# Kernel tuning notes

Measured on AMD Instinct MI355X. Metric: run time of the kernel, lower is better.

Reference implementation:

```python
import jax, jax.numpy as jnp
import numpy as np

N_NODES = 150000  # num_users + num_items
EMB_DIM = 64
N_EDGES = 4000000


def setup_inputs() -> dict:
    key = jax.random.key(0)
    k1, k2 = jax.random.split(key)
    x = jax.random.normal(k1, (N_NODES, EMB_DIM), dtype=jnp.float32)
    edge_index = jax.random.randint(k2, (2, N_EDGES), 0, N_NODES, dtype=jnp.int64)
    return {"x": x, "edge_index": edge_index}


def _lgconv(x, row, col, w):
    # message: x[row] * w ; aggregate: scatter-add into col
    msg = x[row] * w[:, None]  # [E, D]
    return jax.ops.segment_sum(msg, col, num_segments=N_NODES)


def reference(x, edge_index):
    row, col = edge_index[0], edge_index[1]
    # gcn_norm without self-loops: deg from target index (col)
    deg = jax.ops.segment_sum(jnp.ones(row.shape[0], x.dtype), col,
                              num_segments=N_NODES)
    dis = jnp.where(deg > 0, jax.lax.rsqrt(jnp.maximum(deg, 1.0)), 0.0)
    w = dis[row] * dis[col]  # [E]

    emb0 = x
    emb1 = _lgconv(emb0, row, col, w)
    emb2 = _lgconv(emb1, row, col, w)
    # stack over layer dim then mean == mean of the three layer embeddings
    out = (emb0 + emb1 + emb2) / 3.0
    return out
```

## Files before the change

### kernel.cpp

```cpp
#include <hip/hip_runtime.h>
#include <hip/hip_bf16.h>


#define EMB_DIM 64
#define BUCKET_BITS 9
#define BUCKET_SZ 512
#define EPB 8192
#define NBMAX 512
#define CAP 16384
#define GSTRIDE 16

typedef float f32x4 __attribute__((ext_vector_type(4)));

__device__ __forceinline__ float bf_lo(unsigned int q) { return __uint_as_float(q << 16); }
__device__ __forceinline__ float bf_hi(unsigned int q) { return __uint_as_float(q & 0xffff0000u); }
__device__ __forceinline__ unsigned int f2bf(float f) {
    unsigned int u = __float_as_uint(f);
    return (u + 0x7fffu + ((u >> 16) & 1u)) >> 16;
}

__global__ void init_kernel(int* __restrict__ gcur, int NB) {
    int t = threadIdx.x;
    if (t < NB) gcur[t * GSTRIDE] = t * CAP;
}

__global__ void fused_scatter(const int* __restrict__ rows,
                              const int* __restrict__ cols,
                              int* __restrict__ gcur,
                              unsigned int* __restrict__ pairs,
                              int E, int NB) {
    __shared__ unsigned int sbuf[EPB];
    __shared__ unsigned short sbkt[EPB];
    __shared__ int lh[NBMAX];
    __shared__ int lexc[NBMAX];
    __shared__ int lbase[NBMAX];
    __shared__ int lrank[NBMAX];
    __shared__ int sc[NBMAX];
    int blk = blockIdx.x, t = threadIdx.x;
    for (int b = t; b < NBMAX; b += 1024) lh[b] = 0;
    __syncthreads();
    int start = blk * EPB, end = min(start + EPB, E);
    int nloc = end - start;
    int myc[8], myr[8];
#pragma unroll
    for (int j = 0; j < 8; ++j) {
        int i = start + t + j * 1024;
        if (i < end) {
            myc[j] = cols[i];
            myr[j] = rows[i];
            atomicAdd(&lh[myc[j] >> BUCKET_BITS], 1);
        } else {
            myc[j] = -1;
        }
    }
    __syncthreads();
    if (t < NBMAX) sc[t] = lh[t];
    __syncthreads();
    for (int off = 1; off < NBMAX; off <<= 1) {
        int u = (t >= off && t < NBMAX) ? sc[t - off] : 0;
        __syncthreads();
        if (t < NBMAX) sc[t] += u;
        __syncthreads();
    }
    if (t < NBMAX) lexc[t] = sc[t] - lh[t];
    if (t < NB) {
        int c = lh[t];
        lbase[t] = c ? atomicAdd(&gcur[t * GSTRIDE], c) : 0;
        lrank[t] = 0;
    }
    __syncthreads();
#pragma unroll
    for (int j = 0; j < 8; ++j) {
        if (myc[j] >= 0) {
            int b = myc[j] >> BUCKET_BITS;
            int rk = atomicAdd(&lrank[b], 1);
            int p = lexc[b] + rk;
            sbuf[p] = (unsigned)myr[j] |
                      ((unsigned)(myc[j] & (BUCKET_SZ - 1)) << 18);
            sbkt[p] = (unsigned short)b;
        }
    }
    __syncthreads();
    for (int p = t; p < nloc; p += 1024) {
        int b = sbkt[p];
        pairs[lbase[b] + (p - lexc[b])] = sbuf[p];
    }
}

__global__ void count_scan(const int* __restrict__ gcur,
                           int* __restrict__ gbase,
                           int* __restrict__ offsets, int NB, int N, int E) {
    __shared__ int lds[NBMAX];
    int t = threadIdx.x;
    int v = (t < NB) ? (gcur[t * GSTRIDE] - t * CAP) : 0;
    lds[t] = v;
    __syncthreads();
    for (int off = 1; off < NBMAX; off <<= 1) {
        int u = (t >= off) ? lds[t - off] : 0;
        __syncthreads();
        lds[t] += u;
        __syncthreads();
    }
    if (t < NB) gbase[t] = lds[t] - v;
    if (t == 0) offsets[N] = E;
}

__global__ void bucket_finalize(const unsigned int* __restrict__ pairs,
                                const int* __restrict__ gcur,
                                const int* __restrict__ gbase,
                                const float* __restrict__ x,
                                int* __restrict__ edata,
                                int* __restrict__ offsets,
                                float* __restrict__ dis,
                                unsigned short* __restrict__ yb,
                                int N, int E, int NB) {
    __shared__ int ccnt[BUCKET_SZ];
    __shared__ int cexc[BUCKET_SZ];
    __shared__ int sc[1024];
    int b = blockIdx.x, t = threadIdx.x;
    int pbase = b * CAP;
    int cnt = gcur[b * GSTRIDE] - pbase;
    int base = gbase[b];
    int col0 = b << BUCKET_BITS;
    int ncols = min(BUCKET_SZ, N - col0);

    if (t < BUCKET_SZ) ccnt[t] = 0;
    __syncthreads();
    for (int i = t; i < cnt; i += blockDim.x)
        atomicAdd(&ccnt[pairs[pbase + i] >> 18], 1);
    __syncthreads();

    int v = (t < BUCKET_SZ) ? ccnt[t] : 0;
    sc[t] = v;
    __syncthreads();
    for (int off = 1; off < 1024; off <<= 1) {
        int u = (t >= off) ? sc[t - off] : 0;
        __syncthreads();
        sc[t] += u;
        __syncthreads();
    }
    if (t < BUCKET_SZ) cexc[t] = sc[t] - v;
    __syncthreads();

    if (t < ncols) {
        int c = ccnt[t];
        offsets[col0 + t] = base + cexc[t];
        dis[col0 + t] = (c > 0) ? rsqrtf((float)c) : 0.0f;
    }
    if (t < BUCKET_SZ) sc[t] = 0;
    __syncthreads();
    for (int i = t; i < cnt; i += blockDim.x) {
        unsigned p = pairs[pbase + i];
        int lc = p >> 18;
        int src = p & 0x3FFFF;
        int rk = atomicAdd(&sc[lc], 1);
        edata[base + cexc[lc] + rk] = src;
    }

    for (int u = t; u < ncols * 16; u += blockDim.x) {
        int lr = u >> 4;
        int part = u & 15;
        int c = ccnt[lr];
        float d = (c > 0) ? rsqrtf((float)c) : 0.0f;
        size_t o = (((size_t)(col0 + lr)) << 6) + part * 4;
        float4 vx = *(const float4*)(x + o);
        uint2 w;
        w.x = f2bf(vx.x * d) | (f2bf(vx.y * d) << 16);
        w.y = f2bf(vx.z * d) | (f2bf(vx.w * d) << 16);
        *(uint2*)(yb + o) = w;
    }
}

__device__ __forceinline__ void acc8(float* acc, uint4 q) {
    acc[0] += bf_lo(q.x);
    acc[1] += bf_hi(q.x);
    acc[2] += bf_lo(q.y);
    acc[3] += bf_hi(q.y);
    acc[4] += bf_lo(q.z);
    acc[5] += bf_hi(q.z);
    acc[6] += bf_lo(q.w);
    acc[7] += bf_hi(q.w);
}

template <bool FINAL>
__global__ void agg_kernel(const unsigned short* __restrict__ embb,
                           const int* __restrict__ edata,
                           const int* __restrict__ offsets,
                           const float* __restrict__ dis,
                           const float* __restrict__ x,
                           unsigned short* __restrict__ outb,
                           float* __restrict__ outf,
                           int n) {
    int wave = (blockIdx.x * blockDim.x + threadIdx.x) >> 6;
    int lane = threadIdx.x & 63;
    int sub = lane >> 3;
    int dest = (wave << 3) + sub;
    if (dest >= n) return;
    int dimo = (lane & 7) * 8;

    int s = offsets[dest];
    int e = offsets[dest + 1];

    float a0[8] = {0, 0, 0, 0, 0, 0, 0, 0};
    float a1[8] = {0, 0, 0, 0, 0, 0, 0, 0};
    const unsigned short* eb = embb + dimo;

    int k = s;
    int kfull = s + ((e - s) & ~7);
    for (; k < kfull; k += 8) {
        int s0 = edata[k];
        int s1 = edata[k + 1];
        int s2 = edata[k + 2];
        int s3 = edata[k + 3];
        int s4 = edata[k + 4];
        int s5 = edata[k + 5];
        int s6 = edata[k + 6];
        int s7 = edata[k + 7];
        uint4 q0 = *(const uint4*)(eb + ((size_t)s0 << 6));
        uint4 q1 = *(const uint4*)(eb + ((size_t)s1 << 6));
        uint4 q2 = *(const uint4*)(eb + ((size_t)s2 << 6));
        uint4 q3 = *(const uint4*)(eb + ((size_t)s3 << 6));
        uint4 q4 = *(const uint4*)(eb + ((size_t)s4 << 6));
        uint4 q5 = *(const uint4*)(eb + ((size_t)s5 << 6));
        uint4 q6 = *(const uint4*)(eb + ((size_t)s6 << 6));
        uint4 q7 = *(const uint4*)(eb + ((size_t)s7 << 6));
        acc8(a0, q0);
        acc8(a1, q1);
        acc8(a0, q2);
        acc8(a1, q3);
        acc8(a0, q4);
        acc8(a1, q5);
        acc8(a0, q6);
        acc8(a1, q7);
    }
    if (k < e) {
        int s0 = edata[k];
        int s1 = (k + 1 < e) ? edata[k + 1] : -1;
        int s2 = (k + 2 < e) ? edata[k + 2] : -1;
        int s3 = (k + 3 < e) ? edata[k + 3] : -1;
        int s4 = (k + 4 < e) ? edata[k + 4] : -1;
        int s5 = (k + 5 < e) ? edata[k + 5] : -1;
        int s6 = (k + 6 < e) ? edata[k + 6] : -1;
        int s7 = (k + 7 < e) ? edata[k + 7] : -1;
        uint4 q0, q1, q2, q3, q4, q5, q6, q7;
        q0 = *(const uint4*)(eb + ((size_t)s0 << 6));
        if (s1 >= 0) q1 = *(const uint4*)(eb + ((size_t)s1 << 6));
        if (s2 >= 0) q2 = *(const uint4*)(eb + ((size_t)s2 << 6));
        if (s3 >= 0) q3 = *(const uint4*)(eb + ((size_t)s3 << 6));
        if (s4 >= 0) q4 = *(const uint4*)(eb + ((size_t)s4 << 6));
        if (s5 >= 0) q5 = *(const uint4*)(eb + ((size_t)s5 << 6));
        if (s6 >= 0) q6 = *(const uint4*)(eb + ((size_t)s6 << 6));
        if (s7 >= 0) q7 = *(const uint4*)(eb + ((size_t)s7 << 6));
        acc8(a0, q0);
        if (s1 >= 0) acc8(a1, q1);
        if (s2 >= 0) acc8(a0, q2);
        if (s3 >= 0) acc8(a1, q3);
        if (s4 >= 0) acc8(a0, q4);
        if (s5 >= 0) acc8(a1, q5);
        if (s6 >= 0) acc8(a0, q6);
        if (s7 >= 0) acc8(a1, q7);
    }

    float acc[8];
#pragma unroll
    for (int j = 0; j < 8; ++j) acc[j] = a0[j] + a1[j];

    float dc = dis[dest];
    size_t o = ((size_t)dest << 6) + dimo;
    if (FINAL) {
        float rd = (dc > 0.0f) ? 1.0f / dc : 0.0f;
        f32x4 xa = __builtin_nontemporal_load((const f32x4*)(x + o));
        f32x4 xc = __builtin_nontemporal_load((const f32x4*)(x + o) + 1);
        uint4 qz = *(const uint4*)(embb + o);
        const float k3 = 1.0f / 3.0f;
        f32x4 r0, r1;
        r0.x = (xa.x + bf_lo(qz.x) * rd + dc * acc[0]) * k3;
        r0.y = (xa.y + bf_hi(qz.x) * rd + dc * acc[1]) * k3;
        r0.z = (xa.z + bf_lo(qz.y) * rd + dc * acc[2]) * k3;
        r0.w = (xa.w + bf_hi(qz.y) * rd + dc * acc[3]) * k3;
        r1.x = (xc.x + bf_lo(qz.z) * rd + dc * acc[4]) * k3;
        r1.y = (xc.y + bf_hi(qz.z) * rd + dc * acc[5]) * k3;
        r1.z = (xc.z + bf_lo(qz.w) * rd + dc * acc[6]) * k3;
        r1.w = (xc.w + bf_hi(qz.w) * rd + dc * acc[7]) * k3;
        __builtin_nontemporal_store(r0, (f32x4*)(outf + o));
        __builtin_nontemporal_store(r1, (f32x4*)(outf + o) + 1);
    } else {
        float zs = dc * dc;
        uint4 q;
        q.x = f2bf(zs * acc[0]) | (f2bf(zs * acc[1]) << 16);
        q.y = f2bf(zs * acc[2]) | (f2bf(zs * acc[3]) << 16);
        q.z = f2bf(zs * acc[4]) | (f2bf(zs * acc[5]) << 16);
        q.w = f2bf(zs * acc[6]) | (f2bf(zs * acc[7]) << 16);
        *(uint4*)(outb + o) = q;
    }
}

extern "C" void kernel_launch(void* const* d_in, const int* in_sizes, int n_in,
                              void* d_out, int out_size, void* d_ws, size_t ws_size,
                              hipStream_t stream) {
    const float* x  = (const float*)d_in[0];
    const int*   ei = (const int*)d_in[1];
    const int E = in_sizes[1] / 2;
    const int N = in_sizes[0] / EMB_DIM;

    const int* rows = ei;
    const int* cols = ei + E;

    const int NB = (N + BUCKET_SZ - 1) >> BUCKET_BITS;
    const int NBLK = (E + EPB - 1) / EPB;

    int*   gcur    = (int*)d_ws;
    int*   gbase   = gcur + 512 * GSTRIDE;
    float* dis     = (float*)(gbase + 512);
    int*   offsets = (int*)(dis + 150080);
    int*   edata   = offsets + 150080;
    unsigned short* yb = (unsigned short*)(edata + E);
    unsigned short* zb = yb + (size_t)N * EMB_DIM;
    unsigned int* pairs = (unsigned int*)zb;
    float* out = (float*)d_out;

    init_kernel<<<1, 512, 0, stream>>>(gcur, NB);
    fused_scatter<<<NBLK, 1024, 0, stream>>>(rows, cols, gcur, pairs, E, NB);
    count_scan<<<1, 512, 0, stream>>>(gcur, gbase, offsets, NB, N, E);
    bucket_finalize<<<NB, 1024, 0, stream>>>(pairs, gcur, gbase, x, edata,
                                             offsets, dis, yb, N, E, NB);

    int agg_waves = (N + 7) / 8;
    int agg_blocks = (agg_waves + 3) / 4;
    agg_kernel<false><<<agg_blocks, 256, 0, stream>>>(yb, edata, offsets, dis,
                                                      nullptr, zb, nullptr, N);
    agg_kernel<true><<<agg_blocks, 256, 0, stream>>>(zb, edata, offsets, dis,
                                                     x, nullptr, out, N);
}
```

Before: 317.7 us.

## Replace LDS Hillis-Steele scans with wave shuffles, drop count_scan, split yb conversion

The barrier-heavy shared-memory prefix scans in fused_scatter and bucket_finalize become wave-level shuffle scans with a small cross-wave fixup. The separate count_scan launch is removed: each bucket_finalize block sums the preceding bucket counts itself to find its global base. The x-to-bf16 scaling moves out of bucket_finalize into a standalone grid-stride yb_kernel. This cuts barriers and one launch, but adds a redundant prefix read per block and one extra pass over x/dis.

```diff
diff --git a/kernel.cpp b/kernel.cpp
--- a/kernel.cpp
+++ b/kernel.cpp
@@ -19,9 +19,11 @@
     return (u + 0x7fffu + ((u >> 16) & 1u)) >> 16;
 }
 
-__global__ void init_kernel(int* __restrict__ gcur, int NB) {
+__global__ void init_kernel(int* __restrict__ gcur, int* __restrict__ offsets,
+                            int NB, int N, int E) {
     int t = threadIdx.x;
     if (t < NB) gcur[t * GSTRIDE] = t * CAP;
+    if (t == 0) offsets[N] = E;
 }
 
 __global__ void fused_scatter(const int* __restrict__ rows,
@@ -35,7 +37,7 @@
     __shared__ int lexc[NBMAX];
     __shared__ int lbase[NBMAX];
     __shared__ int lrank[NBMAX];
-    __shared__ int sc[NBMAX];
+    __shared__ int wsum[8];
     int blk = blockIdx.x, t = threadIdx.x;
     for (int b = t; b < NBMAX; b += 1024) lh[b] = 0;
     __syncthreads();
@@ -54,15 +56,31 @@
         }
     }
     __syncthreads();
-    if (t < NBMAX) sc[t] = lh[t];
-    __syncthreads();
-    for (int off = 1; off < NBMAX; off <<= 1) {
-        int u = (t >= off && t < NBMAX) ? sc[t - off] : 0;
-        __syncthreads();
-        if (t < NBMAX) sc[t] += u;
-        __syncthreads();
-    }
-    if (t < NBMAX) lexc[t] = sc[t] - lh[t];
+    int v = 0, incl = 0;
+    if (t < 512) {
+        v = lh[t];
+        incl = v;
+        int lane = t & 63;
+#pragma unroll
+        for (int off = 1; off < 64; off <<= 1) {
+            int u = __shfl_up(incl, off, 64);
+            if (lane >= off) incl += u;
+        }
+        if (lane == 63) wsum[t >> 6] = incl;
+    }
+    __syncthreads();
+    if (t < 8) {
+        int s = wsum[t];
+        int inc2 = s;
+#pragma unroll
+        for (int off = 1; off < 8; off <<= 1) {
+            int u = __shfl_up(inc2, off, 64);
+            if (t >= off) inc2 += u;
+        }
+        wsum[t] = inc2 - s;
+    }
+    __syncthreads();
+    if (t < 512) lexc[t] = (incl - v) + wsum[t >> 6];
     if (t < NB) {
         int c = lh[t];
         lbase[t] = c ? atomicAdd(&gcur[t * GSTRIDE], c) : 0;
@@ -87,82 +105,95 @@
     }
 }
 
-__global__ void count_scan(const int* __restrict__ gcur,
-                           int* __restrict__ gbase,
-                           int* __restrict__ offsets, int NB, int N, int E) {
-    __shared__ int lds[NBMAX];
-    int t = threadIdx.x;
-    int v = (t < NB) ? (gcur[t * GSTRIDE] - t * CAP) : 0;
-    lds[t] = v;
-    __syncthreads();
-    for (int off = 1; off < NBMAX; off <<= 1) {
-        int u = (t >= off) ? lds[t - off] : 0;
-        __syncthreads();
-        lds[t] += u;
-        __syncthreads();
-    }
-    if (t < NB) gbase[t] = lds[t] - v;
-    if (t == 0) offsets[N] = E;
-}
-
 __global__ void bucket_finalize(const unsigned int* __restrict__ pairs,
                                 const int* __restrict__ gcur,
-                                const int* __restrict__ gbase,
-                                const float* __restrict__ x,
                                 int* __restrict__ edata,
                                 int* __restrict__ offsets,
                                 float* __restrict__ dis,
-                                unsigned short* __restrict__ yb,
                                 int N, int E, int NB) {
     __shared__ int ccnt[BUCKET_SZ];
     __shared__ int cexc[BUCKET_SZ];
-    __shared__ int sc[1024];
+    __shared__ int rnk[BUCKET_SZ];
+    __shared__ int wsum[16];
+    __shared__ int gb_s;
     int b = blockIdx.x, t = threadIdx.x;
     int pbase = b * CAP;
     int cnt = gcur[b * GSTRIDE] - pbase;
-    int base = gbase[b];
+
+    int part = 0;
+    for (int j = t; j < b; j += 1024) part += gcur[j * GSTRIDE] - j * CAP;
+#pragma unroll
+    for (int off = 32; off; off >>= 1) part += __shfl_down(part, off, 64);
+    if ((t & 63) == 0) wsum[t >> 6] = part;
+    if (t < BUCKET_SZ) ccnt[t] = 0;
+    __syncthreads();
+    if (t == 0) {
+        int g = 0;
+#pragma unroll
+        for (int w = 0; w < 16; ++w) g += wsum[w];
+        gb_s = g;
+    }
+    for (int i = t; i < cnt; i += 1024)
+        atomicAdd(&ccnt[pairs[pbase + i] >> 18], 1);
+    __syncthreads();
+
+    int v = 0, incl = 0;
+    if (t < 512) {
+        v = ccnt[t];
+        incl = v;
+        int lane = t & 63;
+#pragma unroll
+        for (int off = 1; off < 64; off <<= 1) {
+            int u = __shfl_up(incl, off, 64);
+            if (lane >= off) incl += u;
+        }
+        if (lane == 63) wsum[t >> 6] = incl;
+    }
+    __syncthreads();
+    if (t < 8) {
+        int s = wsum[t];
+        int inc2 = s;
+#pragma unroll
+        for (int off = 1; off < 8; off <<= 1) {
+            int u = __shfl_up(inc2, off, 64);
+            if (t >= off) inc2 += u;
+        }
+        wsum[t] = inc2 - s;
+    }
+    __syncthreads();
+    if (t < 512) cexc[t] = (incl - v) + wsum[t >> 6];
+    if (t < BUCKET_SZ) rnk[t] = 0;
+    __syncthreads();
+
+    int base = gb_s;
     int col0 = b << BUCKET_BITS;
     int ncols = min(BUCKET_SZ, N - col0);
-
-    if (t < BUCKET_SZ) ccnt[t] = 0;
-    __syncthreads();
-    for (int i = t; i < cnt; i += blockDim.x)
-        atomicAdd(&ccnt[pairs[pbase + i] >> 18], 1);
-    __syncthreads();
-
-    int v = (t < BUCKET_SZ) ? ccnt[t] : 0;
-    sc[t] = v;
-    __syncthreads();
-    for (int off = 1; off < 1024; off <<= 1) {
-        int u = (t >= off) ? sc[t - off] : 0;
-        __syncthreads();
-        sc[t] += u;
-        __syncthreads();
-    }
-    if (t < BUCKET_SZ) cexc[t] = sc[t] - v;
-    __syncthreads();
-
     if (t < ncols) {
         int c = ccnt[t];
         offsets[col0 + t] = base + cexc[t];
         dis[col0 + t] = (c > 0) ? rsqrtf((float)c) : 0.0f;
     }
-    if (t < BUCKET_SZ) sc[t] = 0;
-    __syncthreads();
-    for (int i = t; i < cnt; i += blockDim.x) {
+    __syncthreads();
+    for (int i = t; i < cnt; i += 1024) {
         unsigned p = pairs[pbase + i];
         int lc = p >> 18;
         int src = p & 0x3FFFF;
-        int rk = atomicAdd(&sc[lc], 1);
+        int rk = atomicAdd(&rnk[lc], 1);
         edata[base + cexc[lc] + rk] = src;
     }
-
-    for (int u = t; u < ncols * 16; u += blockDim.x) {
+}
+
+__global__ void yb_kernel(const float* __restrict__ x,
+                          const float* __restrict__ dis,
+                          unsigned short* __restrict__ yb, int N) {
+    int tid = blockIdx.x * blockDim.x + threadIdx.x;
+    int nth = gridDim.x * blockDim.x;
+    int total = N * 16;
+    for (int u = tid; u < total; u += nth) {
         int lr = u >> 4;
         int part = u & 15;
-        int c = ccnt[lr];
-        float d = (c > 0) ? rsqrtf((float)c) : 0.0f;
-        size_t o = (((size_t)(col0 + lr)) << 6) + part * 4;
+        float d = dis[lr];
+        size_t o = (((size_t)lr) << 6) + part * 4;
         float4 vx = *(const float4*)(x + o);
         uint2 w;
         w.x = f2bf(vx.x * d) | (f2bf(vx.y * d) << 16);
@@ -310,8 +341,7 @@
     const int NBLK = (E + EPB - 1) / EPB;
 
     int*   gcur    = (int*)d_ws;
-    int*   gbase   = gcur + 512 * GSTRIDE;
-    float* dis     = (float*)(gbase + 512);
+    float* dis     = (float*)(gcur + 512 * GSTRIDE);
     int*   offsets = (int*)(dis + 150080);
     int*   edata   = offsets + 150080;
     unsigned short* yb = (unsigned short*)(edata + E);
@@ -319,11 +349,11 @@
     unsigned int* pairs = (unsigned int*)zb;
     float* out = (float*)d_out;
 
-    init_kernel<<<1, 512, 0, stream>>>(gcur, NB);
+    init_kernel<<<1, 512, 0, stream>>>(gcur, offsets, NB, N, E);
     fused_scatter<<<NBLK, 1024, 0, stream>>>(rows, cols, gcur, pairs, E, NB);
-    count_scan<<<1, 512, 0, stream>>>(gcur, gbase, offsets, NB, N, E);
-    bucket_finalize<<<NB, 1024, 0, stream>>>(pairs, gcur, gbase, x, edata,
-                                             offsets, dis, yb, N, E, NB);
+    bucket_finalize<<<NB, 1024, 0, stream>>>(pairs, gcur, edata, offsets,
+                                             dis, N, E, NB);
+    yb_kernel<<<2048, 256, 0, stream>>>(x, dis, yb, N);
 
     int agg_waves = (N + 7) / 8;
     int agg_blocks = (agg_waves + 3) / 4;
```

After: 299.8 us. 5.6% less time.
